# Kernel tuning notes

Hardware: AMD Instinct MI355X
Metric: run time of the kernel (lower is better)

The kernel has to match this reference:

```python
import jax, jax.numpy as jnp
import numpy as np


def setup_inputs() -> dict:
    key = jax.random.key(0)
    kq, kk, kv = jax.random.split(key, 3)
    B, N, M, H, D = 4, 2048, 2048, 8, 64
    queries = jax.random.normal(kq, (B, N, H, D), dtype=jnp.float32)
    keys = jax.random.normal(kk, (B, M, H, D), dtype=jnp.float32)
    values = jax.random.normal(kv, (B, M, H, D), dtype=jnp.float32)
    return {"queries": queries, "keys": keys, "values": values}


def reference(queries, keys, values):
    # queries: [B,N,H,D], keys/values: [B,M,H,D]
    D = queries.shape[3]
    softmax_temp = 1.0 / (D ** 0.5)
    QK = jnp.einsum('bnhd,bmhd->bnmh', queries, keys)  # [B,N,M,H]
    A = jax.nn.softmax(softmax_temp * QK, axis=2)      # softmax over M
    queried_values = jnp.einsum('bnmh,bmhd->bnhd', A, values)
    attention_weight = jnp.transpose(A, (0, 3, 1, 2))  # [B,H,N,M]
    return (queried_values, attention_weight)
```

## Files before the change

### kernel.cpp

```cpp
#include <hip/hip_runtime.h>

typedef __bf16 bf16x8 __attribute__((ext_vector_type(8)));
typedef float floatx4 __attribute__((ext_vector_type(4)));
typedef unsigned short ushort8 __attribute__((ext_vector_type(8)));
typedef unsigned short ushort4v __attribute__((ext_vector_type(4)));

#define MFMA(a, b, c) __builtin_amdgcn_mfma_f32_16x16x32_bf16((a), (b), (c), 0, 0, 0)

__device__ __forceinline__ unsigned short f2bf(float x) {
  union { float f; unsigned u; } v; v.f = x;
  unsigned r = v.u + 0x7FFFu + ((v.u >> 16) & 1u);
  return (unsigned short)(r >> 16);
}

__global__ __launch_bounds__(256)
void prep(const float* __restrict__ K, const float* __restrict__ V,
          unsigned short* __restrict__ Kb, unsigned short* __restrict__ Vt)
{
  __shared__ float Vl[64 * 68];

  const int bx = blockIdx.x;
  const int mt = bx & 31;
  const int bh = bx >> 5;
  const int b  = bh >> 3, h = bh & 7;
  const int tid = threadIdx.x;
  const int r  = tid >> 2;
  const int cq = tid & 3;

  const size_t inbase = ((size_t)(b * 2048 + mt * 64 + r) * 8 + h) * 64 + cq * 16;
  unsigned short* ktile = Kb + ((size_t)bh * 32 + mt) * 4096;
  unsigned short* vtile = Vt + ((size_t)bh * 32 + mt) * 4096;

  {
    float4 a0 = *(const float4*)(K + inbase);
    float4 a1 = *(const float4*)(K + inbase + 4);
    float4 a2 = *(const float4*)(K + inbase + 8);
    float4 a3 = *(const float4*)(K + inbase + 12);
    ushort8 o0 = { f2bf(a0.x), f2bf(a0.y), f2bf(a0.z), f2bf(a0.w),
                   f2bf(a1.x), f2bf(a1.y), f2bf(a1.z), f2bf(a1.w) };
    ushort8 o1 = { f2bf(a2.x), f2bf(a2.y), f2bf(a2.z), f2bf(a2.w),
                   f2bf(a3.x), f2bf(a3.y), f2bf(a3.z), f2bf(a3.w) };
    *(ushort8*)(ktile + r * 64 + (((cq * 2)     ^ (r & 7)) * 8)) = o0;
    *(ushort8*)(ktile + r * 64 + (((cq * 2 + 1) ^ (r & 7)) * 8)) = o1;
  }

  {
    float4 a0 = *(const float4*)(V + inbase);
    float4 a1 = *(const float4*)(V + inbase + 4);
    float4 a2 = *(const float4*)(V + inbase + 8);
    float4 a3 = *(const float4*)(V + inbase + 12);
    float vv[16] = { a0.x,a0.y,a0.z,a0.w, a1.x,a1.y,a1.z,a1.w,
                     a2.x,a2.y,a2.z,a2.w, a3.x,a3.y,a3.z,a3.w };
    #pragma unroll
    for (int j = 0; j < 16; ++j) Vl[(cq * 16 + j) * 68 + r] = vv[j];
  }
  __syncthreads();
  {
    float4 w0 = *(const float4*)&Vl[r * 68 + cq * 16];
    float4 w1 = *(const float4*)&Vl[r * 68 + cq * 16 + 4];
    float4 w2 = *(const float4*)&Vl[r * 68 + cq * 16 + 8];
    float4 w3 = *(const float4*)&Vl[r * 68 + cq * 16 + 12];
    ushort8 p0 = { f2bf(w0.x), f2bf(w0.y), f2bf(w0.z), f2bf(w0.w),
                   f2bf(w1.x), f2bf(w1.y), f2bf(w1.z), f2bf(w1.w) };
    ushort8 p1 = { f2bf(w2.x), f2bf(w2.y), f2bf(w2.z), f2bf(w2.w),
                   f2bf(w3.x), f2bf(w3.y), f2bf(w3.z), f2bf(w3.w) };
    *(ushort8*)(vtile + r * 64 + (((cq * 2)     ^ (r & 7)) * 8)) = p0;
    *(ushort8*)(vtile + r * 64 + (((cq * 2 + 1) ^ (r & 7)) * 8)) = p1;
  }
}

__device__ __forceinline__ void stage1k(const unsigned short* gsrc, unsigned short* lds,
                                        int w, int l)
{
  const char* g = (const char*)gsrc + w * 1024 + l * 16;
  char* sd = (char*)lds + w * 1024;
  __builtin_amdgcn_global_load_lds((const __attribute__((address_space(1))) unsigned int*)g,
                                   (__attribute__((address_space(3))) unsigned int*)sd, 16, 0, 0);
}

__device__ __forceinline__ bf16x8 frag(const unsigned short* lds, int r, int bo)
{
  int slot = ((bo >> 4) ^ r) & 7;
  return *(const bf16x8*)((const char*)lds + r * 128 + (slot << 4));
}

__global__ __launch_bounds__(512, 4)
void attn_fwd(const float* __restrict__ Q, const unsigned short* __restrict__ Kb,
              const unsigned short* __restrict__ Vt,
              float* __restrict__ outQV, float* __restrict__ outA)
{
  __shared__ __align__(16) unsigned short pool[40960];
  unsigned short* Kp = pool;
  unsigned short* Vp = pool + 16384;
  unsigned short* As = pool + 32768;

  const int tid = threadIdx.x;
  const int w  = tid >> 6;
  const int l  = tid & 63;
  const int c  = l & 15;
  const int q4 = l >> 4;

  const int bx = (blockIdx.x & 7) * 64 + (blockIdx.x >> 3);
  const int qt = bx & 15;
  const int bh = bx >> 4;
  const int h  = bh & 7;
  const int b  = bh >> 3;
  const int q0 = qt * 128;

  const float scale = 0.125f * 1.44269504088896340736f;

  const size_t base = (size_t)b * (2048 * 512) + (size_t)h * 64;
  const float* Qb = Q + base + (size_t)q0 * 512;

  const unsigned short* Kt0 = Kb + (size_t)bh * (32 * 4096);
  const unsigned short* Vt0 = Vt + (size_t)bh * (32 * 4096);

  bf16x8 bQ0, bQ1;
  {
    const float* qp = Qb + (size_t)(16 * w + c) * 512 + q4 * 8;
    float4 qa0 = *(const float4*)(qp);
    float4 qa1 = *(const float4*)(qp + 4);
    float4 qb0 = *(const float4*)(qp + 32);
    float4 qb1 = *(const float4*)(qp + 36);
    ushort8 t0, t1;
    t0[0]=f2bf(qa0.x*scale); t0[1]=f2bf(qa0.y*scale); t0[2]=f2bf(qa0.z*scale); t0[3]=f2bf(qa0.w*scale);
    t0[4]=f2bf(qa1.x*scale); t0[5]=f2bf(qa1.y*scale); t0[6]=f2bf(qa1.z*scale); t0[7]=f2bf(qa1.w*scale);
    t1[0]=f2bf(qb0.x*scale); t1[1]=f2bf(qb0.y*scale); t1[2]=f2bf(qb0.z*scale); t1[3]=f2bf(qb0.w*scale);
    t1[4]=f2bf(qb1.x*scale); t1[5]=f2bf(qb1.y*scale); t1[6]=f2bf(qb1.z*scale); t1[7]=f2bf(qb1.w*scale);
    bQ0 = __builtin_bit_cast(bf16x8, t0);
    bQ1 = __builtin_bit_cast(bf16x8, t1);
  }

  stage1k(Kt0,        Kp,        w, l);
  stage1k(Kt0 + 4096, Kp + 4096, w, l);
  asm volatile("s_waitcnt vmcnt(0)" ::: "memory");
  __builtin_amdgcn_s_barrier();
  __builtin_amdgcn_sched_barrier(0);

  float lsum[4] = {0.f, 0.f, 0.f, 0.f};
  for (int s = 0; s < 16; ++s) {
    const int pp = s & 1;
    if (s < 15) {
      stage1k(Kt0 + (size_t)(2 * s + 2) * 4096, Kp + (pp ^ 1) * 8192,        w, l);
      stage1k(Kt0 + (size_t)(2 * s + 3) * 4096, Kp + (pp ^ 1) * 8192 + 4096, w, l);
    }
    __builtin_amdgcn_sched_barrier(0);
    __builtin_amdgcn_s_setprio(1);
    #pragma unroll
    for (int j = 0; j < 2; ++j) {
      const unsigned short* Kc = Kp + (pp * 2 + j) * 4096;
      #pragma unroll
      for (int t = 0; t < 4; ++t) {
        bf16x8 aK0 = frag(Kc, t * 16 + c, q4 * 16);
        bf16x8 aK1 = frag(Kc, t * 16 + c, 64 + q4 * 16);
        floatx4 acc = {0.f, 0.f, 0.f, 0.f};
        acc = MFMA(aK0, bQ0, acc);
        acc = MFMA(aK1, bQ1, acc);
        #pragma unroll
        for (int i = 0; i < 4; ++i) lsum[i] += __builtin_amdgcn_exp2f(acc[i]);
      }
    }
    __builtin_amdgcn_s_setprio(0);
    __builtin_amdgcn_sched_barrier(0);
    asm volatile("s_waitcnt vmcnt(0)" ::: "memory");
    __builtin_amdgcn_s_barrier();
    __builtin_amdgcn_sched_barrier(0);
  }
  float rs = (lsum[0] + lsum[1]) + (lsum[2] + lsum[3]);
  rs += __shfl_xor(rs, 16);
  rs += __shfl_xor(rs, 32);
  const float rcp = 1.0f / rs;

  floatx4 Oacc[4];
  #pragma unroll
  for (int t = 0; t < 4; ++t) Oacc[t] = (floatx4){0.f, 0.f, 0.f, 0.f};

  const int arow = 16 * w + c;
  float* aRowP = outA + (((size_t)bh * 2048 + q0 + arow) * 2048) + q4 * 4;

  stage1k(Kt0,        Kp,        w, l);
  stage1k(Kt0 + 4096, Kp + 4096, w, l);
  stage1k(Vt0,        Vp,        w, l);
  stage1k(Vt0 + 4096, Vp + 4096, w, l);
  asm volatile("s_waitcnt vmcnt(0)" ::: "memory");
  __builtin_amdgcn_s_barrier();
  __builtin_amdgcn_sched_barrier(0);

  for (int s = 0; s < 16; ++s) {
    const int pp = s & 1;
    if (s < 15) {
      stage1k(Kt0 + (size_t)(2 * s + 2) * 4096, Kp + (pp ^ 1) * 8192,        w, l);
      stage1k(Kt0 + (size_t)(2 * s + 3) * 4096, Kp + (pp ^ 1) * 8192 + 4096, w, l);
      stage1k(Vt0 + (size_t)(2 * s + 2) * 4096, Vp + (pp ^ 1) * 8192,        w, l);
      stage1k(Vt0 + (size_t)(2 * s + 3) * 4096, Vp + (pp ^ 1) * 8192 + 4096, w, l);
    }
    __builtin_amdgcn_sched_barrier(0);
    __builtin_amdgcn_s_setprio(1);
    #pragma unroll
    for (int j = 0; j < 2; ++j) {
      const unsigned short* Kc = Kp + (pp * 2 + j) * 4096;
      const unsigned short* Vc = Vp + (pp * 2 + j) * 4096;
      const int mc = (2 * s + j) * 64;
      #pragma unroll
      for (int t = 0; t < 4; ++t) {
        bf16x8 aK0 = frag(Kc, t * 16 + c, q4 * 16);
        bf16x8 aK1 = frag(Kc, t * 16 + c, 64 + q4 * 16);
        floatx4 acc = {0.f, 0.f, 0.f, 0.f};
        acc = MFMA(aK0, bQ0, acc);
        acc = MFMA(aK1, bQ1, acc);
        floatx4 av;
        av[0] = __builtin_amdgcn_exp2f(acc[0]) * rcp;
        av[1] = __builtin_amdgcn_exp2f(acc[1]) * rcp;
        av[2] = __builtin_amdgcn_exp2f(acc[2]) * rcp;
        av[3] = __builtin_amdgcn_exp2f(acc[3]) * rcp;
        *(floatx4*)(aRowP + mc + t * 16) = av;
        ushort4v us = { f2bf(av[0]), f2bf(av[1]), f2bf(av[2]), f2bf(av[3]) };
        int bo = t * 32 + q4 * 8;
        int slot = ((bo >> 4) ^ arow) & 7;
        *(ushort4v*)((char*)As + arow * 128 + (slot << 4) + (bo & 15)) = us;
      }
      {
        int s0 = ((q4) ^ arow) & 7;
        int s1 = ((4 + q4) ^ arow) & 7;
        bf16x8 aP0 = *(const bf16x8*)((const char*)As + arow * 128 + (s0 << 4));
        bf16x8 aP1 = *(const bf16x8*)((const char*)As + arow * 128 + (s1 << 4));
        #pragma unroll
        for (int t = 0; t < 4; ++t) {
          bf16x8 bV0 = frag(Vc, t * 16 + c, q4 * 16);
          bf16x8 bV1 = frag(Vc, t * 16 + c, 64 + q4 * 16);
          Oacc[t] = MFMA(aP0, bV0, Oacc[t]);
          Oacc[t] = MFMA(aP1, bV1, Oacc[t]);
        }
      }
    }
    __builtin_amdgcn_s_setprio(0);
    __builtin_amdgcn_sched_barrier(0);
    asm volatile("s_waitcnt vmcnt(8)" ::: "memory");
    __builtin_amdgcn_s_barrier();
    __builtin_amdgcn_sched_barrier(0);
  }

  #pragma unroll
  for (int t = 0; t < 4; ++t) {
    #pragma unroll
    for (int i = 0; i < 4; ++i) {
      outQV[base + (size_t)(q0 + 16 * w + q4 * 4 + i) * 512 + t * 16 + c] = Oacc[t][i];
    }
  }
}

extern "C" void kernel_launch(void* const* d_in, const int* in_sizes, int n_in,
                              void* d_out, int out_size, void* d_ws, size_t ws_size,
                              hipStream_t stream)
{
  const float* Q = (const float*)d_in[0];
  const float* K = (const float*)d_in[1];
  const float* V = (const float*)d_in[2];
  float* outQV = (float*)d_out;
  float* outA  = (float*)d_out + 4194304;

  unsigned short* Kb = (unsigned short*)d_ws;
  unsigned short* Vt = (unsigned short*)d_ws + 4194304;

  prep<<<dim3(1024), dim3(256), 0, stream>>>(K, V, Kb, Vt);
  attn_fwd<<<dim3(512), dim3(512), 0, stream>>>(Q, Kb, Vt, outQV, outA);
}
```

Baseline: 627.3 us.

## Move softmax row-sum pass into prep kernel running alongside K/V conversion

The first pass of attn_fwd (QK^T plus exp2 to compute row sums) moves into a merged prep kernel. Half of its blocks convert K/V to bf16 tiles and the other half compute row sums straight from fp32 K. The reciprocal sum is stashed in the first element of each outA row, and attn_fwd reads it back before overwriting that row. The intent is to overlap the row-sum pass with the conversion work and shorten the main kernel, at the cost of reading fp32 K twice and relying on outA as scratch.

```diff
diff --git a/kernel.cpp b/kernel.cpp
--- a/kernel.cpp
+++ b/kernel.cpp
@@ -13,59 +13,145 @@
   return (unsigned short)(r >> 16);
 }
 
-__global__ __launch_bounds__(256)
-void prep(const float* __restrict__ K, const float* __restrict__ V,
-          unsigned short* __restrict__ Kb, unsigned short* __restrict__ Vt)
-{
-  __shared__ float Vl[64 * 68];
-
+__device__ __forceinline__ bf16x8 frag(const unsigned short* lds, int r, int bo)
+{
+  int slot = ((bo >> 4) ^ r) & 7;
+  return *(const bf16x8*)((const char*)lds + r * 128 + (slot << 4));
+}
+
+__global__ __launch_bounds__(512, 4)
+void prep_rs(const float* __restrict__ Q, const float* __restrict__ K,
+             const float* __restrict__ V, unsigned short* __restrict__ Kb,
+             unsigned short* __restrict__ Vt, float* __restrict__ outA)
+{
+  __shared__ __align__(16) char smem[34816];
+  const int tid = threadIdx.x;
   const int bx = blockIdx.x;
-  const int mt = bx & 31;
-  const int bh = bx >> 5;
-  const int b  = bh >> 3, h = bh & 7;
-  const int tid = threadIdx.x;
-  const int r  = tid >> 2;
-  const int cq = tid & 3;
-
-  const size_t inbase = ((size_t)(b * 2048 + mt * 64 + r) * 8 + h) * 64 + cq * 16;
-  unsigned short* ktile = Kb + ((size_t)bh * 32 + mt) * 4096;
-  unsigned short* vtile = Vt + ((size_t)bh * 32 + mt) * 4096;
-
-  {
-    float4 a0 = *(const float4*)(K + inbase);
-    float4 a1 = *(const float4*)(K + inbase + 4);
-    float4 a2 = *(const float4*)(K + inbase + 8);
-    float4 a3 = *(const float4*)(K + inbase + 12);
-    ushort8 o0 = { f2bf(a0.x), f2bf(a0.y), f2bf(a0.z), f2bf(a0.w),
-                   f2bf(a1.x), f2bf(a1.y), f2bf(a1.z), f2bf(a1.w) };
-    ushort8 o1 = { f2bf(a2.x), f2bf(a2.y), f2bf(a2.z), f2bf(a2.w),
-                   f2bf(a3.x), f2bf(a3.y), f2bf(a3.z), f2bf(a3.w) };
-    *(ushort8*)(ktile + r * 64 + (((cq * 2)     ^ (r & 7)) * 8)) = o0;
-    *(ushort8*)(ktile + r * 64 + (((cq * 2 + 1) ^ (r & 7)) * 8)) = o1;
-  }
-
-  {
-    float4 a0 = *(const float4*)(V + inbase);
-    float4 a1 = *(const float4*)(V + inbase + 4);
-    float4 a2 = *(const float4*)(V + inbase + 8);
-    float4 a3 = *(const float4*)(V + inbase + 12);
-    float vv[16] = { a0.x,a0.y,a0.z,a0.w, a1.x,a1.y,a1.z,a1.w,
-                     a2.x,a2.y,a2.z,a2.w, a3.x,a3.y,a3.z,a3.w };
-    #pragma unroll
-    for (int j = 0; j < 16; ++j) Vl[(cq * 16 + j) * 68 + r] = vv[j];
-  }
-  __syncthreads();
-  {
-    float4 w0 = *(const float4*)&Vl[r * 68 + cq * 16];
-    float4 w1 = *(const float4*)&Vl[r * 68 + cq * 16 + 4];
-    float4 w2 = *(const float4*)&Vl[r * 68 + cq * 16 + 8];
-    float4 w3 = *(const float4*)&Vl[r * 68 + cq * 16 + 12];
-    ushort8 p0 = { f2bf(w0.x), f2bf(w0.y), f2bf(w0.z), f2bf(w0.w),
-                   f2bf(w1.x), f2bf(w1.y), f2bf(w1.z), f2bf(w1.w) };
-    ushort8 p1 = { f2bf(w2.x), f2bf(w2.y), f2bf(w2.z), f2bf(w2.w),
-                   f2bf(w3.x), f2bf(w3.y), f2bf(w3.z), f2bf(w3.w) };
-    *(ushort8*)(vtile + r * 64 + (((cq * 2)     ^ (r & 7)) * 8)) = p0;
-    *(ushort8*)(vtile + r * 64 + (((cq * 2 + 1) ^ (r & 7)) * 8)) = p1;
+
+  if (bx < 512) {
+    const int sub  = tid >> 8;
+    const int stid = tid & 255;
+    const int bh = bx >> 4;
+    const int mt = (bx & 15) * 2 + sub;
+    const int b  = bh >> 3, h = bh & 7;
+    const int r  = stid >> 2;
+    const int cq = stid & 3;
+    float* Vl = (float*)smem + sub * 4352;
+
+    const size_t inbase = ((size_t)(b * 2048 + mt * 64 + r) * 8 + h) * 64 + cq * 16;
+    unsigned short* ktile = Kb + ((size_t)bh * 32 + mt) * 4096;
+    unsigned short* vtile = Vt + ((size_t)bh * 32 + mt) * 4096;
+
+    {
+      float4 a0 = *(const float4*)(K + inbase);
+      float4 a1 = *(const float4*)(K + inbase + 4);
+      float4 a2 = *(const float4*)(K + inbase + 8);
+      float4 a3 = *(const float4*)(K + inbase + 12);
+      ushort8 o0 = { f2bf(a0.x), f2bf(a0.y), f2bf(a0.z), f2bf(a0.w),
+                     f2bf(a1.x), f2bf(a1.y), f2bf(a1.z), f2bf(a1.w) };
+      ushort8 o1 = { f2bf(a2.x), f2bf(a2.y), f2bf(a2.z), f2bf(a2.w),
+                     f2bf(a3.x), f2bf(a3.y), f2bf(a3.z), f2bf(a3.w) };
+      *(ushort8*)(ktile + r * 64 + (((cq * 2)     ^ (r & 7)) * 8)) = o0;
+      *(ushort8*)(ktile + r * 64 + (((cq * 2 + 1) ^ (r & 7)) * 8)) = o1;
+    }
+    {
+      float4 a0 = *(const float4*)(V + inbase);
+      float4 a1 = *(const float4*)(V + inbase + 4);
+      float4 a2 = *(const float4*)(V + inbase + 8);
+      float4 a3 = *(const float4*)(V + inbase + 12);
+      float vv[16] = { a0.x,a0.y,a0.z,a0.w, a1.x,a1.y,a1.z,a1.w,
+                       a2.x,a2.y,a2.z,a2.w, a3.x,a3.y,a3.z,a3.w };
+      #pragma unroll
+      for (int j = 0; j < 16; ++j) Vl[(cq * 16 + j) * 68 + r] = vv[j];
+    }
+    __syncthreads();
+    {
+      float4 w0 = *(const float4*)&Vl[r * 68 + cq * 16];
+      float4 w1 = *(const float4*)&Vl[r * 68 + cq * 16 + 4];
+      float4 w2 = *(const float4*)&Vl[r * 68 + cq * 16 + 8];
+      float4 w3 = *(const float4*)&Vl[r * 68 + cq * 16 + 12];
+      ushort8 p0 = { f2bf(w0.x), f2bf(w0.y), f2bf(w0.z), f2bf(w0.w),
+                     f2bf(w1.x), f2bf(w1.y), f2bf(w1.z), f2bf(w1.w) };
+      ushort8 p1 = { f2bf(w2.x), f2bf(w2.y), f2bf(w2.z), f2bf(w2.w),
+                     f2bf(w3.x), f2bf(w3.y), f2bf(w3.z), f2bf(w3.w) };
+      *(ushort8*)(vtile + r * 64 + (((cq * 2)     ^ (r & 7)) * 8)) = p0;
+      *(ushort8*)(vtile + r * 64 + (((cq * 2 + 1) ^ (r & 7)) * 8)) = p1;
+    }
+  } else {
+    const int bx2 = bx - 512;
+    const int bh = bx2 >> 4;
+    const int qt = bx2 & 15;
+    const int b  = bh >> 3, h = bh & 7;
+    const int q0 = qt * 128;
+    const int w  = tid >> 6;
+    const int l  = tid & 63;
+    const int c  = l & 15;
+    const int q4 = l >> 4;
+    const float scale = 0.125f * 1.44269504088896340736f;
+
+    const size_t base = (size_t)b * (2048 * 512) + (size_t)h * 64;
+    const float* Qb = Q + base + (size_t)q0 * 512;
+
+    bf16x8 bQ0, bQ1;
+    {
+      const float* qp = Qb + (size_t)(16 * w + c) * 512 + q4 * 8;
+      float4 qa0 = *(const float4*)(qp);
+      float4 qa1 = *(const float4*)(qp + 4);
+      float4 qb0 = *(const float4*)(qp + 32);
+      float4 qb1 = *(const float4*)(qp + 36);
+      ushort8 t0, t1;
+      t0[0]=f2bf(qa0.x*scale); t0[1]=f2bf(qa0.y*scale); t0[2]=f2bf(qa0.z*scale); t0[3]=f2bf(qa0.w*scale);
+      t0[4]=f2bf(qa1.x*scale); t0[5]=f2bf(qa1.y*scale); t0[6]=f2bf(qa1.z*scale); t0[7]=f2bf(qa1.w*scale);
+      t1[0]=f2bf(qb0.x*scale); t1[1]=f2bf(qb0.y*scale); t1[2]=f2bf(qb0.z*scale); t1[3]=f2bf(qb0.w*scale);
+      t1[4]=f2bf(qb1.x*scale); t1[5]=f2bf(qb1.y*scale); t1[6]=f2bf(qb1.z*scale); t1[7]=f2bf(qb1.w*scale);
+      bQ0 = __builtin_bit_cast(bf16x8, t0);
+      bQ1 = __builtin_bit_cast(bf16x8, t1);
+    }
+
+    unsigned short* Kl = (unsigned short*)smem;
+    const int r = tid >> 3;
+    const int e = tid & 7;
+
+    float4 ra, rb;
+    #define LOADK(mtv) do { \
+      const float* p = K + base + (size_t)((mtv) * 64 + r) * 512 + e * 8; \
+      ra = *(const float4*)p; rb = *(const float4*)(p + 4); \
+    } while (0)
+    #define WRITEK(bufsel) do { \
+      ushort8 o = { f2bf(ra.x), f2bf(ra.y), f2bf(ra.z), f2bf(ra.w), \
+                    f2bf(rb.x), f2bf(rb.y), f2bf(rb.z), f2bf(rb.w) }; \
+      *(ushort8*)(Kl + (bufsel) * 4096 + r * 64 + ((e ^ (r & 7)) * 8)) = o; \
+    } while (0)
+
+    LOADK(0);
+    WRITEK(0);
+    __syncthreads();
+
+    float lsum[4] = {0.f, 0.f, 0.f, 0.f};
+    for (int mt = 0; mt < 32; ++mt) {
+      if (mt + 1 < 32) LOADK(mt + 1);
+      const unsigned short* Kc = Kl + (mt & 1) * 4096;
+      #pragma unroll
+      for (int t = 0; t < 4; ++t) {
+        bf16x8 aK0 = frag(Kc, t * 16 + c, q4 * 16);
+        bf16x8 aK1 = frag(Kc, t * 16 + c, 64 + q4 * 16);
+        floatx4 acc = {0.f, 0.f, 0.f, 0.f};
+        acc = MFMA(aK0, bQ0, acc);
+        acc = MFMA(aK1, bQ1, acc);
+        #pragma unroll
+        for (int i = 0; i < 4; ++i) lsum[i] += __builtin_amdgcn_exp2f(acc[i]);
+      }
+      if (mt + 1 < 32) WRITEK((mt & 1) ^ 1);
+      __syncthreads();
+    }
+    #undef LOADK
+    #undef WRITEK
+
+    float rs = (lsum[0] + lsum[1]) + (lsum[2] + lsum[3]);
+    rs += __shfl_xor(rs, 16);
+    rs += __shfl_xor(rs, 32);
+    if (q4 == 0)
+      outA[((size_t)(bh * 2048) + q0 + 16 * w + c) * 2048] = 1.0f / rs;
   }
 }
 
@@ -76,12 +162,6 @@
   char* sd = (char*)lds + w * 1024;
   __builtin_amdgcn_global_load_lds((const __attribute__((address_space(1))) unsigned int*)g,
                                    (__attribute__((address_space(3))) unsigned int*)sd, 16, 0, 0);
-}
-
-__device__ __forceinline__ bf16x8 frag(const unsigned short* lds, int r, int bo)
-{
-  int slot = ((bo >> 4) ^ r) & 7;
-  return *(const bf16x8*)((const char*)lds + r * 128 + (slot << 4));
 }
 
 __global__ __launch_bounds__(512, 4)
@@ -114,6 +194,9 @@
 
   const unsigned short* Kt0 = Kb + (size_t)bh * (32 * 4096);
   const unsigned short* Vt0 = Vt + (size_t)bh * (32 * 4096);
+
+  const int arow = 16 * w + c;
+  const float rcp = outA[((size_t)(bh * 2048) + q0 + arow) * 2048];
 
   bf16x8 bQ0, bQ1;
   {
@@ -131,51 +214,10 @@
     bQ1 = __builtin_bit_cast(bf16x8, t1);
   }
 
-  stage1k(Kt0,        Kp,        w, l);
-  stage1k(Kt0 + 4096, Kp + 4096, w, l);
-  asm volatile("s_waitcnt vmcnt(0)" ::: "memory");
-  __builtin_amdgcn_s_barrier();
-  __builtin_amdgcn_sched_barrier(0);
-
-  float lsum[4] = {0.f, 0.f, 0.f, 0.f};
-  for (int s = 0; s < 16; ++s) {
-    const int pp = s & 1;
-    if (s < 15) {
-      stage1k(Kt0 + (size_t)(2 * s + 2) * 4096, Kp + (pp ^ 1) * 8192,        w, l);
-      stage1k(Kt0 + (size_t)(2 * s + 3) * 4096, Kp + (pp ^ 1) * 8192 + 4096, w, l);
-    }
-    __builtin_amdgcn_sched_barrier(0);
-    __builtin_amdgcn_s_setprio(1);
-    #pragma unroll
-    for (int j = 0; j < 2; ++j) {
-      const unsigned short* Kc = Kp + (pp * 2 + j) * 4096;
-      #pragma unroll
-      for (int t = 0; t < 4; ++t) {
-        bf16x8 aK0 = frag(Kc, t * 16 + c, q4 * 16);
-        bf16x8 aK1 = frag(Kc, t * 16 + c, 64 + q4 * 16);
-        floatx4 acc = {0.f, 0.f, 0.f, 0.f};
-        acc = MFMA(aK0, bQ0, acc);
-        acc = MFMA(aK1, bQ1, acc);
-        #pragma unroll
-        for (int i = 0; i < 4; ++i) lsum[i] += __builtin_amdgcn_exp2f(acc[i]);
-      }
-    }
-    __builtin_amdgcn_s_setprio(0);
-    __builtin_amdgcn_sched_barrier(0);
-    asm volatile("s_waitcnt vmcnt(0)" ::: "memory");
-    __builtin_amdgcn_s_barrier();
-    __builtin_amdgcn_sched_barrier(0);
-  }
-  float rs = (lsum[0] + lsum[1]) + (lsum[2] + lsum[3]);
-  rs += __shfl_xor(rs, 16);
-  rs += __shfl_xor(rs, 32);
-  const float rcp = 1.0f / rs;
-
   floatx4 Oacc[4];
   #pragma unroll
   for (int t = 0; t < 4; ++t) Oacc[t] = (floatx4){0.f, 0.f, 0.f, 0.f};
 
-  const int arow = 16 * w + c;
   float* aRowP = outA + (((size_t)bh * 2048 + q0 + arow) * 2048) + q4 * 4;
 
   stage1k(Kt0,        Kp,        w, l);
@@ -262,6 +304,6 @@
   unsigned short* Kb = (unsigned short*)d_ws;
   unsigned short* Vt = (unsigned short*)d_ws + 4194304;
 
-  prep<<<dim3(1024), dim3(256), 0, stream>>>(K, V, Kb, Vt);
+  prep_rs<<<dim3(1024), dim3(512), 0, stream>>>(Q, K, V, Kb, Vt, outA);
   attn_fwd<<<dim3(512), dim3(512), 0, stream>>>(Q, Kb, Vt, outQV, outA);
 }
```

Result: no change. 639.8 us (+2.0%).
